# Kernel tuning notes

Measured on AMD Instinct MI355X. Metric: run time of the kernel, lower is better.

## Reference

```python
import jax, jax.numpy as jnp
import numpy as np

D_MODEL = 2048
N_HEADS = 16
HEAD_DIM = D_MODEL // N_HEADS
ROPE_BASE = 10000.0


def rope(x):
    # x: [b, h, s, d]; matches the torch module exactly:
    # x1 = even dims, x2 = odd dims; output = concat([x1*cos - x2*sin, x1*sin + x2*cos], -1)
    b, h, s, d = x.shape
    theta = 1.0 / ROPE_BASE ** (jnp.arange(0, d, 2, dtype=jnp.float32) / d)  # [d/2]
    angles = jnp.arange(s, dtype=jnp.float32)[:, None] * theta[None, :]       # [s, d/2]
    cos = jnp.cos(angles)[None, None]  # [1,1,s,d/2]
    sin = jnp.sin(angles)[None, None]
    x1, x2 = x[..., ::2], x[..., 1::2]
    return jnp.concatenate([x1 * cos - x2 * sin, x1 * sin + x2 * cos], axis=-1)


def setup_inputs() -> dict:
    key = jax.random.key(0)
    ks = jax.random.split(key, 5)
    b, s = 2, 2048
    x = jax.random.normal(ks[0], (b, s, D_MODEL), dtype=jnp.float32)
    scale_in = 1.0 / np.sqrt(D_MODEL)
    Wqkv = jax.random.normal(ks[1], (D_MODEL, 3 * D_MODEL), dtype=jnp.float32) * scale_in
    bqkv = jnp.zeros((3 * D_MODEL,), dtype=jnp.float32)
    Wo = jax.random.normal(ks[2], (D_MODEL, D_MODEL), dtype=jnp.float32) * scale_in
    bo = jnp.zeros((D_MODEL,), dtype=jnp.float32)
    return {"x": x, "Wqkv": Wqkv, "bqkv": bqkv, "Wo": Wo, "bo": bo}


def reference(x, Wqkv, bqkv, Wo, bo):
    b, s, d = x.shape
    qkv = x @ Wqkv + bqkv                      # [b, s, 3d]
    q, k, v = jnp.split(qkv, 3, axis=-1)
    def to_heads(t):
        return t.reshape(b, s, N_HEADS, HEAD_DIM).transpose(0, 2, 1, 3)  # [b,h,s,hd]
    q, k, v = to_heads(q), to_heads(k), to_heads(v)
    q = rope(q)
    k = rope(k)
    scores = jnp.einsum('bhqd,bhkd->bhqk', q, k) / jnp.sqrt(jnp.float32(HEAD_DIM))
    attn = jax.nn.softmax(scores, axis=-1)
    out = jnp.einsum('bhqk,bhkd->bhqd', attn, v)
    out = out.transpose(0, 2, 1, 3).reshape(b, s, d)
    return out @ Wo + bo
```

## Files before the change

kernel.cpp:

```cpp
#include <hip/hip_runtime.h>
#include <hip/hip_bf16.h>
#include <cstdint>
#include <type_traits>

#define D_MODEL 2048
#define NH 16
#define HD 128
#define SEQ 2048
#define QKV_LD (3 * D_MODEL)

typedef __attribute__((ext_vector_type(8))) short short8;
typedef __attribute__((ext_vector_type(4))) float f32x4;
typedef __attribute__((ext_vector_type(16))) float f32x16;

__device__ __forceinline__ ushort f2bf(float f) {
    union { float f; uint32_t u; } c; c.f = f;
    uint32_t u = c.u;
    uint32_t r = (u + 0x7FFFu + ((u >> 16) & 1u)) >> 16;
    return (ushort)r;
}
__device__ __forceinline__ float bf2f(ushort b) {
    union { uint32_t u; float f; } c; c.u = ((uint32_t)b) << 16;
    return c.f;
}

__device__ __forceinline__ void load_lds16(const ushort* g, ushort* l) {
    __builtin_amdgcn_global_load_lds(
        (const __attribute__((address_space(1))) void*)g,
        (__attribute__((address_space(3))) void*)l, 16, 0, 0);
}

__global__ void cvt_bf16_kernel(const float* __restrict__ in, ushort* __restrict__ out, int n4) {
    int idx = blockIdx.x * blockDim.x + threadIdx.x;
    if (idx >= n4) return;
    float4 v = ((const float4*)in)[idx];
    ushort4 o;
    o.x = f2bf(v.x); o.y = f2bf(v.y); o.z = f2bf(v.z); o.w = f2bf(v.w);
    ((ushort4*)out)[idx] = o;
}

__global__ void transpose_bf16_kernel(const float* __restrict__ in, ushort* __restrict__ out,
                                      int R, int C) {
    __shared__ float tile[32][33];
    int tx = threadIdx.x, ty = threadIdx.y;
    int c0 = blockIdx.x * 32, r0 = blockIdx.y * 32;
    for (int i = 0; i < 4; ++i) {
        int r = r0 + ty + i * 8;
        tile[ty + i * 8][tx] = in[(size_t)r * C + c0 + tx];
    }
    __syncthreads();
    for (int i = 0; i < 4; ++i) {
        int c = c0 + ty + i * 8;
        out[(size_t)c * R + r0 + tx] = f2bf(tile[tx][ty + i * 8]);
    }
}

#define WAITV(N) asm volatile("s_waitcnt vmcnt(" #N ")" ::: "memory")
#define LGKM0()  do { asm volatile("s_waitcnt lgkmcnt(0)" ::: "memory"); \
                      __builtin_amdgcn_sched_barrier(0); } while (0)
#define BAR()    do { __builtin_amdgcn_s_barrier(); \
                      __builtin_amdgcn_sched_barrier(0); } while (0)

#define STAGE_A(L, T_, B_) load_lds16(Ag + (size_t)(L) * 64 * K + (size_t)(T_) * 64, \
                                      smA + (B_) * 16384 + (L) * 4096 + ldsW)
#define STAGE_B(L, T_, B_) load_lds16(Bg + (size_t)(((L) & 1) * 128 + ((L) >> 1) * 32) * K + (size_t)(T_) * 64, \
                                      smB + (B_) * 16384 + (L) * 4096 + ldsW)
#define READ_A(MH) do { const ushort* _ab = smA + cb * 16384 + aRow + (MH) * 4096; \
    _Pragma("unroll") for (int i_ = 0; i_ < 4; ++i_) { \
        af[i_][0] = *(const short8*)(_ab + i_ * 1024 + pc0); \
        af[i_][1] = *(const short8*)(_ab + i_ * 1024 + pc1); } } while (0)
#define READ_B(NHh) do { const ushort* _bb = smB + cb * 16384 + (NHh) * 8192 + bRow; \
    _Pragma("unroll") for (int j_ = 0; j_ < 2; ++j_) { \
        bfr[j_][0] = *(const short8*)(_bb + j_ * 1024 + pc0); \
        bfr[j_][1] = *(const short8*)(_bb + j_ * 1024 + pc1); } } while (0)
#define MFMA16(MH, NHh) do { \
    _Pragma("unroll") for (int i_ = 0; i_ < 4; ++i_) \
    _Pragma("unroll") for (int j_ = 0; j_ < 2; ++j_) { \
        acc[(MH) * 4 + i_][(NHh) * 2 + j_] = __builtin_amdgcn_mfma_f32_16x16x32_bf16( \
            af[i_][0], bfr[j_][0], acc[(MH) * 4 + i_][(NHh) * 2 + j_], 0, 0, 0); \
        acc[(MH) * 4 + i_][(NHh) * 2 + j_] = __builtin_amdgcn_mfma_f32_16x16x32_bf16( \
            af[i_][1], bfr[j_][1], acc[(MH) * 4 + i_][(NHh) * 2 + j_], 0, 0, 0); } } while (0)

template <typename OutT>
__global__ __launch_bounds__(512, 2) void gemm256(
    const ushort* __restrict__ A,
    const ushort* __restrict__ Bt,
    const float* __restrict__ bias,
    OutT* __restrict__ C,
    int M, int N, int K)
{
    __shared__ __align__(16) ushort sm[65536];
    ushort* smA = sm;
    ushort* smB = sm + 32768;

    int t = threadIdx.x;
    int w = t >> 6, lane = t & 63;
    int lr = lane & 15, lh = lane >> 4;
    int wm_idx = w >> 2, wn_idx = w & 3;
    int m0 = blockIdx.y * 256, n0 = blockIdx.x * 256;

    int srow = t >> 3;
    int scol = ((t & 7) ^ (srow & 7)) << 3;
    const ushort* Ag = A + (size_t)(m0 + srow) * K + scol;
    int bq = (srow >> 5) * 64 + (srow & 31);
    const ushort* Bg = Bt + (size_t)(n0 + bq) * K + scol;
    int ldsW = w * 512;

    int pc0 = (lh ^ (lr & 7)) << 3;
    int pc1 = ((4 + lh) ^ (lr & 7)) << 3;
    int aRow = (wm_idx * 128 + lr) * 64;
    int bRow = (wn_idx * 32 + lr) * 64;

    f32x4 acc[8][4];
#pragma unroll
    for (int i = 0; i < 8; ++i)
#pragma unroll
        for (int j = 0; j < 4; ++j) acc[i][j] = (f32x4)0.0f;
    short8 af[4][2], bfr[2][2];

    int NT = K >> 6;

    STAGE_A(0, 0, 0); STAGE_A(2, 0, 0); STAGE_B(0, 0, 0); STAGE_B(1, 0, 0);
    STAGE_B(2, 0, 0); STAGE_B(3, 0, 0);
    STAGE_A(1, 0, 0); STAGE_A(3, 0, 0);
    WAITV(4);
    BAR();

    for (int T = 0; T < NT; ++T) {
        int cb = T & 1, nb = cb ^ 1;
        bool pf = (T + 1 < NT);
        READ_A(0); READ_B(0);
        if (pf) { STAGE_A(0, T + 1, nb); STAGE_A(2, T + 1, nb);
                  STAGE_B(0, T + 1, nb); STAGE_B(1, T + 1, nb); }
        BAR(); LGKM0();
        __builtin_amdgcn_s_setprio(1); MFMA16(0, 0); __builtin_amdgcn_s_setprio(0);
        if (pf) WAITV(6); else WAITV(2);
        BAR();
        READ_B(1);
        if (pf) { STAGE_B(2, T + 1, nb); STAGE_B(3, T + 1, nb); }
        BAR(); LGKM0();
        __builtin_amdgcn_s_setprio(1); MFMA16(0, 1); __builtin_amdgcn_s_setprio(0);
        if (pf) WAITV(6); else WAITV(0);
        BAR();
        READ_A(1);
        if (pf) { STAGE_A(1, T + 1, nb); STAGE_A(3, T + 1, nb); }
        BAR(); LGKM0();
        __builtin_amdgcn_s_setprio(1); MFMA16(1, 1); __builtin_amdgcn_s_setprio(0);
        BAR();
        READ_B(0);
        BAR(); LGKM0();
        __builtin_amdgcn_s_setprio(1); MFMA16(1, 0); __builtin_amdgcn_s_setprio(0);
        WAITV(4);
        BAR();
    }

    float bv[4];
#pragma unroll
    for (int jj = 0; jj < 4; ++jj) bv[jj] = bias[n0 + wn_idx * 64 + jj * 16 + lr];
#pragma unroll
    for (int ii = 0; ii < 8; ++ii) {
        int row = m0 + wm_idx * 128 + ii * 16 + lh * 4;
#pragma unroll
        for (int jj = 0; jj < 4; ++jj) {
            int col = n0 + wn_idx * 64 + jj * 16 + lr;
#pragma unroll
            for (int r = 0; r < 4; ++r) {
                float v = acc[ii][jj][r] + bv[jj];
                if constexpr (std::is_same<OutT, ushort>::value)
                    C[(size_t)(row + r) * N + col] = f2bf(v);
                else
                    C[(size_t)(row + r) * N + col] = v;
            }
        }
    }
}

__global__ void rope_table(float2* __restrict__ tab) {
    int i = blockIdx.x * blockDim.x + threadIdx.x;
    int s = i >> 6, j = i & 63;
    float theta = powf(10000.0f, -(float)j * (1.0f / 64.0f));
    float ang = (float)s * theta;
    float sn, cs;
    sincosf(ang, &sn, &cs);
    tab[i] = make_float2(cs, sn);
}

__global__ void rope_cast_qk(const ushort* __restrict__ qkv,
                             const float2* __restrict__ tab,
                             ushort* __restrict__ Qb, ushort* __restrict__ Kb) {
    int t = threadIdx.x;
    int wv = blockIdx.x * 4 + (t >> 6);
    int j = t & 63;
    int bs = wv >> 5;
    int rem = wv & 31;
    int which = rem >> 4;
    int h = rem & 15;
    int s = bs & 2047;
    int b = bs >> 11;
    size_t src = (size_t)bs * QKV_LD + which * D_MODEL + h * HD;
    uint32_t pr = *(const uint32_t*)(qkv + src + 2 * j);
    float x1 = bf2f((ushort)(pr & 0xffff));
    float x2 = bf2f((ushort)(pr >> 16));
    float2 cspair = tab[(s << 6) + j];
    float cs = cspair.x, sn = cspair.y;
    float sc = which ? 1.0f : 0.08838834764831845f;
    float o1 = (x1 * cs - x2 * sn) * sc;
    float o2 = (x1 * sn + x2 * cs) * sc;
    ushort* dst = which ? Kb : Qb;
    size_t obase = ((size_t)(b * NH + h) * SEQ + s) * HD;
    dst[obase + j] = f2bf(o1);
    dst[obase + 64 + j] = f2bf(o2);
}

__global__ void v_transpose(const ushort* __restrict__ qkv, ushort* __restrict__ Vt) {
    __shared__ ushort tile[32][33];
    int tx = threadIdx.x, ty = threadIdx.y;
    int s0 = blockIdx.x * 32;
    int d0 = blockIdx.y * 32;
    int bh = blockIdx.z;
    int b = bh >> 4, h = bh & 15;
    for (int i = 0; i < 4; ++i) {
        int s = s0 + ty + i * 8;
        tile[ty + i * 8][tx] = qkv[((size_t)(b * SEQ + s)) * QKV_LD + 2 * D_MODEL + h * HD + d0 + tx];
    }
    __syncthreads();
    for (int i = 0; i < 4; ++i) {
        int d = d0 + ty + i * 8;
        Vt[((size_t)bh * HD + d) * SEQ + s0 + tx] = tile[tx][ty + i * 8];
    }
}

__global__ __launch_bounds__(256) void attn_mfma(const ushort* __restrict__ Qb,
                                                 const ushort* __restrict__ Kb,
                                                 const ushort* __restrict__ Vt,
                                                 ushort* __restrict__ ctx) {
    __shared__ ushort smem[25600];
    ushort* Ks = smem;
    ushort* Vts = smem + 8192;
    ushort* Ps = smem + 16384;

    int t = threadIdx.x;
    int w = t >> 6, l = t & 63;
    int l31 = l & 31, g = l >> 5;
    int q0 = blockIdx.x * 128;
    int bh = blockIdx.y;
    int b = bh >> 4, h = bh & 15;

    int qrow = q0 + w * 32 + l31;
    const ushort* Qg = Qb + ((size_t)bh * SEQ + qrow) * HD;
    short8 qf[8];
#pragma unroll
    for (int kc = 0; kc < 8; kc++)
        qf[kc] = *(const short8*)(Qg + kc * 16 + g * 8);

    f32x16 O[4];
#pragma unroll
    for (int di = 0; di < 4; di++) O[di] = (f32x16)0.0f;
    float m_run = -INFINITY, l_run = 0.0f;

    const ushort* KgB = Kb + (size_t)bh * SEQ * HD;
    const ushort* VtB = Vt + (size_t)bh * HD * SEQ;

    for (int k0 = 0; k0 < SEQ; k0 += 64) {
        __syncthreads();
#pragma unroll
        for (int c2 = 0; c2 < 4; c2++) {
            int f = c2 * 256 + t;
            int r = f >> 4, c = f & 15;
            int cp = c ^ (r & 15);
            uint4 v = *(const uint4*)(KgB + (size_t)(k0 + r) * HD + c * 8);
            *(uint4*)(Ks + r * 128 + cp * 8) = v;
        }
#pragma unroll
        for (int c2 = 0; c2 < 4; c2++) {
            int f = c2 * 256 + t;
            int d = f >> 3, c = f & 7;
            int cp = c ^ (d & 7);
            uint4 v = *(const uint4*)(VtB + (size_t)d * SEQ + k0 + c * 8);
            *(uint4*)(Vts + d * 64 + cp * 8) = v;
        }
        __syncthreads();

        f32x16 St[2];
        St[0] = (f32x16)0.0f;
        St[1] = (f32x16)0.0f;
#pragma unroll
        for (int ki = 0; ki < 2; ki++) {
            int row = ki * 32 + l31;
#pragma unroll
            for (int kc = 0; kc < 8; kc++) {
                int cp = (kc * 2 + g) ^ (row & 15);
                short8 a = *(const short8*)(Ks + row * 128 + cp * 8);
                St[ki] = __builtin_amdgcn_mfma_f32_32x32x16_bf16(a, qf[kc], St[ki], 0, 0, 0);
            }
        }

        float mx = -INFINITY;
#pragma unroll
        for (int ki = 0; ki < 2; ki++)
#pragma unroll
            for (int r = 0; r < 16; r++) mx = fmaxf(mx, St[ki][r]);
        mx = fmaxf(mx, __shfl_xor(mx, 32));
        float mn = fmaxf(m_run, mx);
        float alpha = __expf(m_run - mn);
        m_run = mn;
        float psum = 0.0f;
#pragma unroll
        for (int ki = 0; ki < 2; ki++)
#pragma unroll
            for (int r = 0; r < 16; r++) {
                float p = __expf(St[ki][r] - mn);
                St[ki][r] = p;
                psum += p;
            }
        psum += __shfl_xor(psum, 32);
        l_run = l_run * alpha + psum;
#pragma unroll
        for (int di = 0; di < 4; di++)
#pragma unroll
            for (int r = 0; r < 16; r++) O[di][r] *= alpha;

        {
            int qloc = w * 32 + l31;
            ushort* Pr = Ps + qloc * 72;
#pragma unroll
            for (int ki = 0; ki < 2; ki++)
#pragma unroll
                for (int u = 0; u < 4; u++) {
                    ushort4 pk;
                    pk.x = f2bf(St[ki][4 * u + 0]);
                    pk.y = f2bf(St[ki][4 * u + 1]);
                    pk.z = f2bf(St[ki][4 * u + 2]);
                    pk.w = f2bf(St[ki][4 * u + 3]);
                    *(ushort4*)(Pr + ki * 32 + 8 * u + 4 * g) = pk;
                }
        }

        {
            int qloc = w * 32 + l31;
            short8 pb[4];
#pragma unroll
            for (int kc = 0; kc < 4; kc++)
                pb[kc] = *(const short8*)(Ps + qloc * 72 + kc * 16 + g * 8);
#pragma unroll
            for (int di = 0; di < 4; di++) {
                int d = di * 32 + l31;
#pragma unroll
                for (int kc = 0; kc < 4; kc++) {
                    int cp = (kc * 2 + g) ^ (d & 7);
                    short8 va = *(const short8*)(Vts + d * 64 + cp * 8);
                    O[di] = __builtin_amdgcn_mfma_f32_32x32x16_bf16(va, pb[kc], O[di], 0, 0, 0);
                }
            }
        }
    }

    __syncthreads();
    float inv = 1.0f / l_run;
    ushort* ob = smem;
    {
        int qloc = w * 32 + l31;
        ushort* orow = ob + qloc * 128;
#pragma unroll
        for (int di = 0; di < 4; di++)
#pragma unroll
            for (int u = 0; u < 4; u++) {
                ushort4 pk;
                pk.x = f2bf(O[di][4 * u + 0] * inv);
                pk.y = f2bf(O[di][4 * u + 1] * inv);
                pk.z = f2bf(O[di][4 * u + 2] * inv);
                pk.w = f2bf(O[di][4 * u + 3] * inv);
                *(ushort4*)(orow + di * 32 + 8 * u + 4 * g) = pk;
            }
    }
#pragma unroll
    for (int p = 0; p < 8; p++) {
        int qloc = w * 32 + p * 4 + (l >> 4);
        int c16 = l & 15;
        uint4 v = *(const uint4*)(ob + qloc * 128 + c16 * 8);
        size_t tok = (size_t)b * SEQ + q0 + qloc;
        *(uint4*)(ctx + tok * D_MODEL + h * HD + c16 * 8) = v;
    }
}

extern "C" void kernel_launch(void* const* d_in, const int* in_sizes, int n_in,
                              void* d_out, int out_size, void* d_ws, size_t ws_size,
                              hipStream_t stream) {
    const float* x    = (const float*)d_in[0];
    const float* Wqkv = (const float*)d_in[1];
    const float* bqkv = (const float*)d_in[2];
    const float* Wo   = (const float*)d_in[3];
    const float* bo   = (const float*)d_in[4];
    float* out = (float*)d_out;

    char* ws = (char*)d_ws;
    ushort* x_bf   = (ushort*)(ws);
    ushort* wqkvT  = (ushort*)(ws + 16777216);
    ushort* woT    = (ushort*)(ws + 41943040);
    ushort* qkv_bf = (ushort*)(ws + 50331648);
    ushort* Qb     = (ushort*)(ws + 100663296);
    ushort* Kb     = (ushort*)(ws + 117440512);
    ushort* VtG    = (ushort*)(ws + 134217728);
    ushort* ctx    = (ushort*)(ws + 150994944);
    float2* rtab   = (float2*)(ws + 150994944);

    rope_table<<<512, 256, 0, stream>>>(rtab);
    cvt_bf16_kernel<<<8192, 256, 0, stream>>>(x, x_bf, 2097152);
    transpose_bf16_kernel<<<dim3(192, 64), dim3(32, 8), 0, stream>>>(Wqkv, wqkvT, 2048, 6144);
    transpose_bf16_kernel<<<dim3(64, 64), dim3(32, 8), 0, stream>>>(Wo, woT, 2048, 2048);
    gemm256<ushort><<<dim3(24, 16), 512, 0, stream>>>(x_bf, wqkvT, bqkv, qkv_bf, 4096, 6144, 2048);
    rope_cast_qk<<<32768, 256, 0, stream>>>(qkv_bf, rtab, Qb, Kb);
    v_transpose<<<dim3(64, 4, 32), dim3(32, 8), 0, stream>>>(qkv_bf, VtG);
    attn_mfma<<<dim3(16, 32), 256, 0, stream>>>(Qb, Kb, VtG, ctx);
    gemm256<float><<<dim3(8, 16), 512, 0, stream>>>(ctx, woT, bo, out, 4096, 2048, 2048);
}
```

Before: 447.2 us.

## Template GEMM on N-tile width, use 256x128 tiles for output projection

```diff
diff --git a/kernel.cpp b/kernel.cpp
--- a/kernel.cpp
+++ b/kernel.cpp
@@ -56,32 +56,33 @@
 }
 
 #define WAITV(N) asm volatile("s_waitcnt vmcnt(" #N ")" ::: "memory")
-#define LGKM0()  do { asm volatile("s_waitcnt lgkmcnt(0)" ::: "memory"); \
-                      __builtin_amdgcn_sched_barrier(0); } while (0)
-#define BAR()    do { __builtin_amdgcn_s_barrier(); \
-                      __builtin_amdgcn_sched_barrier(0); } while (0)
-
+#define BARF()   do { __builtin_amdgcn_s_barrier(); \
+                      asm volatile("" ::: "memory"); } while (0)
+#define PRIO1    __builtin_amdgcn_s_setprio(1)
+#define PRIO0    __builtin_amdgcn_s_setprio(0)
+
+#define B_ROWOFF(L) (NHALF == 2 ? (((L) & 1) * 128 + ((L) >> 1) * 32) : ((L) * 64))
 #define STAGE_A(L, T_, B_) load_lds16(Ag + (size_t)(L) * 64 * K + (size_t)(T_) * 64, \
                                       smA + (B_) * 16384 + (L) * 4096 + ldsW)
-#define STAGE_B(L, T_, B_) load_lds16(Bg + (size_t)(((L) & 1) * 128 + ((L) >> 1) * 32) * K + (size_t)(T_) * 64, \
-                                      smB + (B_) * 16384 + (L) * 4096 + ldsW)
+#define STAGE_B(L, T_, B_) load_lds16(Bg + (size_t)B_ROWOFF(L) * K + (size_t)(T_) * 64, \
+                                      smB + (B_) * (8192 * NHALF) + (L) * 4096 + ldsW)
 #define READ_A(MH) do { const ushort* _ab = smA + cb * 16384 + aRow + (MH) * 4096; \
     _Pragma("unroll") for (int i_ = 0; i_ < 4; ++i_) { \
         af[i_][0] = *(const short8*)(_ab + i_ * 1024 + pc0); \
         af[i_][1] = *(const short8*)(_ab + i_ * 1024 + pc1); } } while (0)
-#define READ_B(NHh) do { const ushort* _bb = smB + cb * 16384 + (NHh) * 8192 + bRow; \
+#define READ_BH(dst, NHh) do { const ushort* _bb = smB + cb * (8192 * NHALF) + (NHh) * 8192 + bRow; \
     _Pragma("unroll") for (int j_ = 0; j_ < 2; ++j_) { \
-        bfr[j_][0] = *(const short8*)(_bb + j_ * 1024 + pc0); \
-        bfr[j_][1] = *(const short8*)(_bb + j_ * 1024 + pc1); } } while (0)
-#define MFMA16(MH, NHh) do { \
+        dst[j_][0] = *(const short8*)(_bb + j_ * 1024 + pc0); \
+        dst[j_][1] = *(const short8*)(_bb + j_ * 1024 + pc1); } } while (0)
+#define MFMA_PH(MH, NHh, bf) do { \
     _Pragma("unroll") for (int i_ = 0; i_ < 4; ++i_) \
     _Pragma("unroll") for (int j_ = 0; j_ < 2; ++j_) { \
         acc[(MH) * 4 + i_][(NHh) * 2 + j_] = __builtin_amdgcn_mfma_f32_16x16x32_bf16( \
-            af[i_][0], bfr[j_][0], acc[(MH) * 4 + i_][(NHh) * 2 + j_], 0, 0, 0); \
+            af[i_][0], bf[j_][0], acc[(MH) * 4 + i_][(NHh) * 2 + j_], 0, 0, 0); \
         acc[(MH) * 4 + i_][(NHh) * 2 + j_] = __builtin_amdgcn_mfma_f32_16x16x32_bf16( \
-            af[i_][1], bfr[j_][1], acc[(MH) * 4 + i_][(NHh) * 2 + j_], 0, 0, 0); } } while (0)
-
-template <typename OutT>
+            af[i_][1], bf[j_][1], acc[(MH) * 4 + i_][(NHh) * 2 + j_], 0, 0, 0); } } while (0)
+
+template <typename OutT, int NHALF>
 __global__ __launch_bounds__(512, 2) void gemm256(
     const ushort* __restrict__ A,
     const ushort* __restrict__ Bt,
@@ -89,7 +90,7 @@
     OutT* __restrict__ C,
     int M, int N, int K)
 {
-    __shared__ __align__(16) ushort sm[65536];
+    __shared__ __align__(16) ushort sm[32768 + 2 * 8192 * NHALF];
     ushort* smA = sm;
     ushort* smB = sm + 32768;
 
@@ -97,12 +98,12 @@
     int w = t >> 6, lane = t & 63;
     int lr = lane & 15, lh = lane >> 4;
     int wm_idx = w >> 2, wn_idx = w & 3;
-    int m0 = blockIdx.y * 256, n0 = blockIdx.x * 256;
+    int m0 = blockIdx.y * 256, n0 = blockIdx.x * (128 * NHALF);
 
     int srow = t >> 3;
     int scol = ((t & 7) ^ (srow & 7)) << 3;
     const ushort* Ag = A + (size_t)(m0 + srow) * K + scol;
-    int bq = (srow >> 5) * 64 + (srow & 31);
+    int bq = (NHALF == 2) ? ((srow >> 5) * 64 + (srow & 31)) : srow;
     const ushort* Bg = Bt + (size_t)(n0 + bq) * K + scol;
     int ldsW = w * 512;
 
@@ -111,58 +112,75 @@
     int aRow = (wm_idx * 128 + lr) * 64;
     int bRow = (wn_idx * 32 + lr) * 64;
 
-    f32x4 acc[8][4];
+    f32x4 acc[8][2 * NHALF];
 #pragma unroll
     for (int i = 0; i < 8; ++i)
 #pragma unroll
-        for (int j = 0; j < 4; ++j) acc[i][j] = (f32x4)0.0f;
-    short8 af[4][2], bfr[2][2];
+        for (int j = 0; j < 2 * NHALF; ++j) acc[i][j] = (f32x4)0.0f;
+    short8 af[4][2], bf0[2][2], bf1[2][2];
 
     int NT = K >> 6;
 
-    STAGE_A(0, 0, 0); STAGE_A(2, 0, 0); STAGE_B(0, 0, 0); STAGE_B(1, 0, 0);
-    STAGE_B(2, 0, 0); STAGE_B(3, 0, 0);
-    STAGE_A(1, 0, 0); STAGE_A(3, 0, 0);
-    WAITV(4);
-    BAR();
+    if constexpr (NHALF == 2) {
+        STAGE_A(0, 0, 0); STAGE_A(2, 0, 0); STAGE_B(0, 0, 0); STAGE_B(1, 0, 0);
+        STAGE_B(2, 0, 0); STAGE_B(3, 0, 0);
+        STAGE_A(1, 0, 0); STAGE_A(3, 0, 0);
+        WAITV(4);
+    } else {
+        STAGE_A(0, 0, 0); STAGE_A(2, 0, 0); STAGE_B(0, 0, 0);
+        STAGE_B(1, 0, 0); STAGE_A(1, 0, 0); STAGE_A(3, 0, 0);
+        WAITV(2);
+    }
+    BARF();
 
     for (int T = 0; T < NT; ++T) {
         int cb = T & 1, nb = cb ^ 1;
         bool pf = (T + 1 < NT);
-        READ_A(0); READ_B(0);
-        if (pf) { STAGE_A(0, T + 1, nb); STAGE_A(2, T + 1, nb);
-                  STAGE_B(0, T + 1, nb); STAGE_B(1, T + 1, nb); }
-        BAR(); LGKM0();
-        __builtin_amdgcn_s_setprio(1); MFMA16(0, 0); __builtin_amdgcn_s_setprio(0);
-        if (pf) WAITV(6); else WAITV(2);
-        BAR();
-        READ_B(1);
-        if (pf) { STAGE_B(2, T + 1, nb); STAGE_B(3, T + 1, nb); }
-        BAR(); LGKM0();
-        __builtin_amdgcn_s_setprio(1); MFMA16(0, 1); __builtin_amdgcn_s_setprio(0);
-        if (pf) WAITV(6); else WAITV(0);
-        BAR();
-        READ_A(1);
-        if (pf) { STAGE_A(1, T + 1, nb); STAGE_A(3, T + 1, nb); }
-        BAR(); LGKM0();
-        __builtin_amdgcn_s_setprio(1); MFMA16(1, 1); __builtin_amdgcn_s_setprio(0);
-        BAR();
-        READ_B(0);
-        BAR(); LGKM0();
-        __builtin_amdgcn_s_setprio(1); MFMA16(1, 0); __builtin_amdgcn_s_setprio(0);
-        WAITV(4);
-        BAR();
-    }
-
-    float bv[4];
-#pragma unroll
-    for (int jj = 0; jj < 4; ++jj) bv[jj] = bias[n0 + wn_idx * 64 + jj * 16 + lr];
+        if constexpr (NHALF == 2) {
+            READ_A(0); READ_BH(bf0, 0);
+            if (pf) { STAGE_A(0, T + 1, nb); STAGE_A(2, T + 1, nb);
+                      STAGE_B(0, T + 1, nb); STAGE_B(1, T + 1, nb); }
+            BARF();
+            PRIO1; MFMA_PH(0, 0, bf0); PRIO0;
+            if (pf) WAITV(6); else WAITV(2);
+            BARF();
+            READ_BH(bf1, 1);
+            if (pf) { STAGE_B(2, T + 1, nb); STAGE_B(3, T + 1, nb); }
+            BARF();
+            PRIO1; MFMA_PH(0, 1, bf1); PRIO0;
+            if (pf) WAITV(6); else WAITV(0);
+            BARF();
+            READ_A(1);
+            if (pf) { STAGE_A(1, T + 1, nb); STAGE_A(3, T + 1, nb); }
+            BARF();
+            PRIO1; MFMA_PH(1, 1, bf1); MFMA_PH(1, 0, bf0); PRIO0;
+            if (pf) WAITV(4);
+            BARF();
+        } else {
+            READ_A(0); READ_BH(bf0, 0);
+            if (pf) { STAGE_A(0, T + 1, nb); STAGE_A(2, T + 1, nb); STAGE_B(0, T + 1, nb); }
+            BARF();
+            PRIO1; MFMA_PH(0, 0, bf0); PRIO0;
+            if (pf) WAITV(3); else WAITV(0);
+            BARF();
+            READ_A(1);
+            if (pf) { STAGE_B(1, T + 1, nb); STAGE_A(1, T + 1, nb); STAGE_A(3, T + 1, nb); }
+            BARF();
+            PRIO1; MFMA_PH(1, 0, bf0); PRIO0;
+            if (pf) WAITV(2);
+            BARF();
+        }
+    }
+
+    float bv[2 * NHALF];
+#pragma unroll
+    for (int jj = 0; jj < 2 * NHALF; ++jj) bv[jj] = bias[n0 + wn_idx * 32 * NHALF + jj * 16 + lr];
 #pragma unroll
     for (int ii = 0; ii < 8; ++ii) {
         int row = m0 + wm_idx * 128 + ii * 16 + lh * 4;
 #pragma unroll
-        for (int jj = 0; jj < 4; ++jj) {
-            int col = n0 + wn_idx * 64 + jj * 16 + lr;
+        for (int jj = 0; jj < 2 * NHALF; ++jj) {
+            int col = n0 + wn_idx * 32 * NHALF + jj * 16 + lr;
 #pragma unroll
             for (int r = 0; r < 4; ++r) {
                 float v = acc[ii][jj][r] + bv[jj];
@@ -408,9 +426,9 @@
     cvt_bf16_kernel<<<8192, 256, 0, stream>>>(x, x_bf, 2097152);
     transpose_bf16_kernel<<<dim3(192, 64), dim3(32, 8), 0, stream>>>(Wqkv, wqkvT, 2048, 6144);
     transpose_bf16_kernel<<<dim3(64, 64), dim3(32, 8), 0, stream>>>(Wo, woT, 2048, 2048);
-    gemm256<ushort><<<dim3(24, 16), 512, 0, stream>>>(x_bf, wqkvT, bqkv, qkv_bf, 4096, 6144, 2048);
+    gemm256<ushort, 2><<<dim3(24, 16), 512, 0, stream>>>(x_bf, wqkvT, bqkv, qkv_bf, 4096, 6144, 2048);
     rope_cast_qk<<<32768, 256, 0, stream>>>(qkv_bf, rtab, Qb, Kb);
     v_transpose<<<dim3(64, 4, 32), dim3(32, 8), 0, stream>>>(qkv_bf, VtG);
     attn_mfma<<<dim3(16, 32), 256, 0, stream>>>(Qb, Kb, VtG, ctx);
-    gemm256<float><<<dim3(8, 16), 512, 0, stream>>>(ctx, woT, bo, out, 4096, 2048, 2048);
-}
+    gemm256<float, 1><<<dim3(16, 16), 512, 0, stream>>>(ctx, woT, bo, out, 4096, 2048, 2048);
+}
```

Result: faster. 430.6 us (-3.7%).
